# Performance work log

Hardware: AMD Instinct MI355X
Metric: run time of the kernel (lower is better)

## Reference

```python
import jax, jax.numpy as jnp
import numpy as np

K = 25          # moving-average kernel_size
P = 24          # periodicity
PAD_LEN = 5     # median padding window (padding_mode='median')


def setup_inputs() -> dict:
    key = jax.random.key(0)
    x = jax.random.normal(key, (64, 128, 8192), dtype=jnp.float32)
    return {"x": x}


def _decompose(x):
    B, C, L = x.shape
    half = (K - 1) // 2  # 12

    # --- moving_average_decomposition with 'median' padding ---
    # torch.median over an odd window (5) == jnp.median
    front = jnp.median(x[:, :, :PAD_LEN], axis=2, keepdims=True)   # [B,C,1]
    end = jnp.median(x[:, :, -PAD_LEN:], axis=2, keepdims=True)    # [B,C,1]
    xp = jnp.concatenate(
        [jnp.repeat(front, half, axis=2), x, jnp.repeat(end, half, axis=2)],
        axis=2,
    )  # [B,C,L+K-1]

    # AvgPool1d(kernel=K, stride=1) via prefix-sum difference (single pass)
    cs = jnp.cumsum(xp, axis=-1)
    cs = jnp.concatenate([jnp.zeros_like(cs[:, :, :1]), cs], axis=-1)
    trend = (cs[:, :, K:] - cs[:, :, :-K]) / K                      # [B,C,L]
    res = x - trend

    # --- per-phase seasonal mean (vectorized replacement of python loop) ---
    pad_len = L % P
    if pad_len > 0:
        # original: cat(res, res[:, :, -P:-pad_len]) -> length divisible by P
        xpad = jnp.concatenate([res, res[:, :, -P:-pad_len]], axis=-1)
    else:
        xpad = res
    n = xpad.shape[-1] // P
    # mean over occurrences of each phase i (== mean of x_padded[:, :, i::P])
    seasonal = jnp.mean(xpad.reshape(B, C, n, P), axis=2)           # [B,C,P]
    out_seasonal = jnp.tile(seasonal, (1, 1, n))[:, :, :L]          # broadcast back
    out_residual = res - out_seasonal
    return out_residual, trend, out_seasonal


def reference(x):
    return _decompose(x)
```

## Files before the change

kernel.cpp:

```cpp
#include <hip/hip_runtime.h>
#include <cstdint>

namespace {
constexpr int LROW   = 8192;
constexpr int KWIN   = 25;
constexpr int HALF   = (KWIN - 1) / 2;
constexpr int PERIOD = 24;
constexpr int NOCC   = 342;
constexpr int NTHR   = 256;
constexpr int GRP    = LROW / (4 * NTHR);
}

typedef float f32x4 __attribute__((ext_vector_type(4)));

__device__ __forceinline__ void ce(float& x, float& y) {
    float lo = fminf(x, y), hi = fmaxf(x, y);
    x = lo; y = hi;
}

__device__ __forceinline__ float median5(float a, float b, float c, float d, float e) {
    ce(a, b); ce(d, e); ce(c, e); ce(c, d); ce(a, d); ce(a, c);
    ce(b, e); ce(b, d); ce(b, c);
    return c;
}

__global__ __launch_bounds__(NTHR, 5) void decomp_kernel(
    const float* __restrict__ x,
    float* __restrict__ out_res,
    float* __restrict__ out_trend,
    float* __restrict__ out_seas)
{
    __shared__ __align__(16) float xs[LROW];

    const int t = threadIdx.x;
    const size_t base = (size_t)blockIdx.x * LROW;
    const float* xr = x + base;

    #pragma unroll
    for (int j = 0; j < GRP; ++j) {
        int g = 4 * (t + NTHR * j);
        f32x4 f = __builtin_nontemporal_load(
            reinterpret_cast<const f32x4*>(xr + g));
        *reinterpret_cast<f32x4*>(xs + g) = f;
    }
    __syncthreads();

    float resv[GRP][4];
    #pragma unroll
    for (int j = 0; j < GRP; ++j) {
        int g = 4 * (t + NTHR * j);
        float v[28];
        if (g >= HALF && g <= LROW - 16) {
            #pragma unroll
            for (int q = 0; q < 7; ++q) {
                f32x4 f = *reinterpret_cast<const f32x4*>(xs + g - HALF + 4 * q);
                v[4*q+0] = f.x; v[4*q+1] = f.y; v[4*q+2] = f.z; v[4*q+3] = f.w;
            }
        } else {
            float med = (g < HALF)
                ? median5(xs[0], xs[1], xs[2], xs[3], xs[4])
                : median5(xs[LROW-5], xs[LROW-4], xs[LROW-3], xs[LROW-2], xs[LROW-1]);
            #pragma unroll
            for (int q = 0; q < 28; ++q) {
                int idx = g - HALF + q;
                v[q] = (idx < 0 || idx >= LROW) ? med : xs[idx];
            }
        }
        float s = 0.f;
        #pragma unroll
        for (int q = 0; q < KWIN; ++q) s += v[q];
        constexpr float inv = 1.0f / (float)KWIN;
        float w1 = s  - v[0] + v[25];
        float w2 = w1 - v[1] + v[26];
        float w3 = w2 - v[2] + v[27];
        float t0 = s * inv, t1 = w1 * inv, t2 = w2 * inv, t3 = w3 * inv;
        resv[j][0] = v[12] - t0;
        resv[j][1] = v[13] - t1;
        resv[j][2] = v[14] - t2;
        resv[j][3] = v[15] - t3;
        f32x4 tv; tv.x = t0; tv.y = t1; tv.z = t2; tv.w = t3;
        __builtin_nontemporal_store(
            tv, reinterpret_cast<f32x4*>(out_trend + base + g));
    }
    __syncthreads();

    #pragma unroll
    for (int j = 0; j < GRP; ++j) {
        int g = 4 * (t + NTHR * j);
        f32x4 rv; rv.x = resv[j][0]; rv.y = resv[j][1];
        rv.z = resv[j][2]; rv.w = resv[j][3];
        *reinterpret_cast<f32x4*>(xs + g) = rv;
    }
    __syncthreads();

    float acc = 0.f;
    if (t < 240) {
        const int p = t / 10, s0 = t % 10;
        for (int k = s0; k < NOCC; k += 10) {
            int m = PERIOD * k + p;
            if (m >= LROW) m -= PERIOD;
            acc += xs[m];
        }
    }
    __syncthreads();
    if (t < 240) xs[t] = acc;
    __syncthreads();
    if (t < PERIOD) {
        float s = 0.f;
        #pragma unroll
        for (int q = 0; q < 10; ++q) s += xs[t * 10 + q];
        xs[240 + t] = s / (float)NOCC;
    }
    __syncthreads();

    #pragma unroll
    for (int j = 0; j < GRP; ++j) {
        int g = 4 * (t + NTHR * j);
        int ph = g % PERIOD;
        f32x4 sv = *reinterpret_cast<const f32x4*>(xs + 240 + ph);
        __builtin_nontemporal_store(
            sv, reinterpret_cast<f32x4*>(out_seas + base + g));
        f32x4 rv;
        rv.x = resv[j][0] - sv.x; rv.y = resv[j][1] - sv.y;
        rv.z = resv[j][2] - sv.z; rv.w = resv[j][3] - sv.w;
        __builtin_nontemporal_store(
            rv, reinterpret_cast<f32x4*>(out_res + base + g));
    }
}

extern "C" void kernel_launch(void* const* d_in, const int* in_sizes, int n_in,
                              void* d_out, int out_size, void* d_ws, size_t ws_size,
                              hipStream_t stream) {
    const float* x = (const float*)d_in[0];
    float* out = (float*)d_out;
    const size_t n = (size_t)in_sizes[0];
    const int rows = (int)(n / (size_t)LROW);
    decomp_kernel<<<rows, NTHR, 0, stream>>>(x, out, out + n, out + 2 * n);
}
```

Baseline: 214.5 us.

## Read sliding windows directly from global memory instead of staging in LDS

Removes the initial copy of each row into shared memory and computes the moving-average windows with overlapping vector loads from global memory. This relies on the caches to absorb the reuse. It also switches nontemporal stores to regular stores, lowers the occupancy hint in launch bounds, and moves the partial seasonal sums into separate small LDS arrays so one barrier can be dropped. The trade-off is more global load instructions and cache pressure in exchange for less LDS traffic and fewer barriers.

```diff
diff --git a/kernel.cpp b/kernel.cpp
--- a/kernel.cpp
+++ b/kernel.cpp
@@ -24,26 +24,19 @@
     return c;
 }
 
-__global__ __launch_bounds__(NTHR, 5) void decomp_kernel(
+__global__ __launch_bounds__(NTHR, 4) void decomp_kernel(
     const float* __restrict__ x,
     float* __restrict__ out_res,
     float* __restrict__ out_trend,
     float* __restrict__ out_seas)
 {
     __shared__ __align__(16) float xs[LROW];
+    __shared__ float part[240];
+    __shared__ float seasonal[PERIOD];
 
     const int t = threadIdx.x;
     const size_t base = (size_t)blockIdx.x * LROW;
     const float* xr = x + base;
-
-    #pragma unroll
-    for (int j = 0; j < GRP; ++j) {
-        int g = 4 * (t + NTHR * j);
-        f32x4 f = __builtin_nontemporal_load(
-            reinterpret_cast<const f32x4*>(xr + g));
-        *reinterpret_cast<f32x4*>(xs + g) = f;
-    }
-    __syncthreads();
 
     float resv[GRP][4];
     #pragma unroll
@@ -53,17 +46,17 @@
         if (g >= HALF && g <= LROW - 16) {
             #pragma unroll
             for (int q = 0; q < 7; ++q) {
-                f32x4 f = *reinterpret_cast<const f32x4*>(xs + g - HALF + 4 * q);
+                f32x4 f = *reinterpret_cast<const f32x4*>(xr + g - HALF + 4 * q);
                 v[4*q+0] = f.x; v[4*q+1] = f.y; v[4*q+2] = f.z; v[4*q+3] = f.w;
             }
         } else {
             float med = (g < HALF)
-                ? median5(xs[0], xs[1], xs[2], xs[3], xs[4])
-                : median5(xs[LROW-5], xs[LROW-4], xs[LROW-3], xs[LROW-2], xs[LROW-1]);
+                ? median5(xr[0], xr[1], xr[2], xr[3], xr[4])
+                : median5(xr[LROW-5], xr[LROW-4], xr[LROW-3], xr[LROW-2], xr[LROW-1]);
             #pragma unroll
             for (int q = 0; q < 28; ++q) {
                 int idx = g - HALF + q;
-                v[q] = (idx < 0 || idx >= LROW) ? med : xs[idx];
+                v[q] = (idx < 0 || idx >= LROW) ? med : xr[idx];
             }
         }
         float s = 0.f;
@@ -79,37 +72,29 @@
         resv[j][2] = v[14] - t2;
         resv[j][3] = v[15] - t3;
         f32x4 tv; tv.x = t0; tv.y = t1; tv.z = t2; tv.w = t3;
-        __builtin_nontemporal_store(
-            tv, reinterpret_cast<f32x4*>(out_trend + base + g));
-    }
-    __syncthreads();
-
-    #pragma unroll
-    for (int j = 0; j < GRP; ++j) {
-        int g = 4 * (t + NTHR * j);
+        *reinterpret_cast<f32x4*>(out_trend + base + g) = tv;
         f32x4 rv; rv.x = resv[j][0]; rv.y = resv[j][1];
         rv.z = resv[j][2]; rv.w = resv[j][3];
         *reinterpret_cast<f32x4*>(xs + g) = rv;
     }
     __syncthreads();
 
-    float acc = 0.f;
     if (t < 240) {
         const int p = t / 10, s0 = t % 10;
+        float acc = 0.f;
         for (int k = s0; k < NOCC; k += 10) {
             int m = PERIOD * k + p;
             if (m >= LROW) m -= PERIOD;
             acc += xs[m];
         }
+        part[t] = acc;
     }
-    __syncthreads();
-    if (t < 240) xs[t] = acc;
     __syncthreads();
     if (t < PERIOD) {
         float s = 0.f;
         #pragma unroll
-        for (int q = 0; q < 10; ++q) s += xs[t * 10 + q];
-        xs[240 + t] = s / (float)NOCC;
+        for (int q = 0; q < 10; ++q) s += part[t * 10 + q];
+        seasonal[t] = s / (float)NOCC;
     }
     __syncthreads();
 
@@ -117,14 +102,16 @@
     for (int j = 0; j < GRP; ++j) {
         int g = 4 * (t + NTHR * j);
         int ph = g % PERIOD;
-        f32x4 sv = *reinterpret_cast<const f32x4*>(xs + 240 + ph);
-        __builtin_nontemporal_store(
-            sv, reinterpret_cast<f32x4*>(out_seas + base + g));
+        float s0 = seasonal[ph + 0];
+        float s1 = seasonal[ph + 1];
+        float s2 = seasonal[ph + 2];
+        float s3 = seasonal[ph + 3];
+        f32x4 sv; sv.x = s0; sv.y = s1; sv.z = s2; sv.w = s3;
+        *reinterpret_cast<f32x4*>(out_seas + base + g) = sv;
         f32x4 rv;
-        rv.x = resv[j][0] - sv.x; rv.y = resv[j][1] - sv.y;
-        rv.z = resv[j][2] - sv.z; rv.w = resv[j][3] - sv.w;
-        __builtin_nontemporal_store(
-            rv, reinterpret_cast<f32x4*>(out_res + base + g));
+        rv.x = resv[j][0] - s0; rv.y = resv[j][1] - s1;
+        rv.z = resv[j][2] - s2; rv.w = resv[j][3] - s3;
+        *reinterpret_cast<f32x4*>(out_res + base + g) = rv;
     }
 }
 
```

After: 223.1 us. 4.0% more time.
